# Kernel tuning notes

Hardware: AMD Instinct MI355X
Metric: run time of the kernel (lower is better)

The kernel has to match this reference:

```python
import jax, jax.numpy as jnp
import numpy as np

B, S, D = 1, 2048, 1024
H = 16            # num_heads
DH = D // H       # head dim = 64
WIN = 128         # local window size
DIL = 4           # dilation rate


def setup_inputs() -> dict:
    key = jax.random.key(0)
    k1, k2, k3 = jax.random.split(key, 3)
    x = jax.random.normal(k1, (B, S, D), jnp.float32)
    w_qkv = jax.random.normal(k2, (D, 3 * D), jnp.float32) * 0.02
    w_out = jax.random.normal(k3, (D, D), jnp.float32) * 0.02
    return {"x": x, "w_qkv": w_qkv, "w_out": w_out}


def reference(x, w_qkv, w_out):
    b, s, d = x.shape
    scale = 1.0 / np.sqrt(DH).astype(np.float32)

    qkv = x @ w_qkv                                   # [B,S,3D]
    q, k, v = jnp.split(qkv, 3, axis=-1)
    q = q.reshape(b, s, H, DH)
    k = k.reshape(b, s, H, DH)
    v = v.reshape(b, s, H, DH)

    # ---- local window attention: attend within non-overlapping windows ----
    nw = s // WIN
    qw = q.reshape(b, nw, WIN, H, DH)
    kw = k.reshape(b, nw, WIN, H, DH)
    vw = v.reshape(b, nw, WIN, H, DH)
    s_loc = jnp.einsum('bnihd,bnjhd->bnhij', qw, kw) * scale
    p_loc = jax.nn.softmax(s_loc, axis=-1)
    o_loc = jnp.einsum('bnhij,bnjhd->bnihd', p_loc, vw).reshape(b, s, H, DH)

    # ---- dilated attention: attend within each stride-DIL residue class ----
    n = s // DIL
    # seq index = i*DIL + g  -> position i within dilation group g
    qd = q.reshape(b, n, DIL, H, DH)
    kd = k.reshape(b, n, DIL, H, DH)
    vd = v.reshape(b, n, DIL, H, DH)
    s_dil = jnp.einsum('bighd,bjghd->bghij', qd, kd) * scale
    p_dil = jax.nn.softmax(s_dil, axis=-1)
    o_dil = jnp.einsum('bghij,bjghd->bighd', p_dil, vd).reshape(b, s, H, DH)

    # ---- global full attention ----
    s_glb = jnp.einsum('bihd,bjhd->bhij', q, k) * scale
    p_glb = jax.nn.softmax(s_glb, axis=-1)
    o_glb = jnp.einsum('bhij,bjhd->bihd', p_glb, v)

    # fuse the three scales (uniform average) and project out
    o = (o_loc + o_dil + o_glb) * (1.0 / 3.0)
    return o.reshape(b, s, d) @ w_out
```

## Files before the change

kernel.cpp:

```cpp
#include <hip/hip_runtime.h>
#include <hip/hip_bf16.h>


typedef __attribute__((ext_vector_type(8))) short s8v;
typedef __attribute__((ext_vector_type(4))) float f4v;

#define QSCALE 0.18033688011112042f

__device__ __forceinline__ short f2bf(float f) {
  union { float f; unsigned u; } x; x.f = f;
  unsigned r = (x.u + 0x7FFF + ((x.u >> 16) & 1)) >> 16;
  return (short)r;
}
__device__ __forceinline__ float bf2f(short s) {
  union { unsigned u; float f; } x; x.u = ((unsigned)(unsigned short)s) << 16;
  return x.f;
}
__device__ __forceinline__ f4v mfma16(s8v a, s8v b, f4v c) {
  return __builtin_amdgcn_mfma_f32_16x16x32_bf16(a, b, c, 0, 0, 0);
}
__device__ __forceinline__ void load_lds16(const void* g, void* l) {
  __builtin_amdgcn_global_load_lds(
      (const __attribute__((address_space(1))) unsigned int*)g,
      (__attribute__((address_space(3))) unsigned int*)l, 16, 0, 0);
}
__device__ __forceinline__ float exp2f_fast(float x) {
  return __builtin_amdgcn_exp2f(x);
}

__global__ __launch_bounds__(256)
void fill_const_kernel(float* __restrict__ out, int n, float v) {
  int i = blockIdx.x * 256 + threadIdx.x;
  if (i < n) out[i] = v;
}

__global__ __launch_bounds__(256)
void cast_f32_bf16(const float* __restrict__ src, short* __restrict__ dst, int n) {
  int i = (blockIdx.x * 256 + threadIdx.x) * 4;
  if (i < n) {
    float4 v = *reinterpret_cast<const float4*>(&src[i]);
    union { short s[4]; int2 p; } u;
    u.s[0] = f2bf(v.x); u.s[1] = f2bf(v.y); u.s[2] = f2bf(v.z); u.s[3] = f2bf(v.w);
    *reinterpret_cast<int2*>(&dst[i]) = u.p;
  }
}

__global__ __launch_bounds__(256)
void transpose_conv(const float* __restrict__ src, short* __restrict__ dst,
                    int K, int N) {
  __shared__ float T[64][69];
  const int n0 = blockIdx.x * 64, k0 = blockIdx.y * 64;
  const int t = threadIdx.x;
  for (int jb = t; jb < 1024; jb += 256) {
    int r = jb >> 4, c4 = (jb & 15) * 4;
    float4 v = *reinterpret_cast<const float4*>(&src[(size_t)(k0 + r) * N + n0 + c4]);
    T[c4 + 0][r] = v.x; T[c4 + 1][r] = v.y; T[c4 + 2][r] = v.z; T[c4 + 3][r] = v.w;
  }
  __syncthreads();
  for (int jb = t; jb < 512; jb += 256) {
    int n = jb >> 3, k8 = (jb & 7) * 8;
    union { short s[8]; int4 v; } p;
#pragma unroll
    for (int i = 0; i < 8; ++i) p.s[i] = f2bf(T[n][k8 + i]);
    *reinterpret_cast<int4*>(&dst[(size_t)(n0 + n) * K + k0 + k8]) = p.v;
  }
}

template <int COUT, bool AF32, int NT>
__global__ __launch_bounds__(256)
void gemm_tile(const void* __restrict__ Av, const short* __restrict__ Bt,
               short* __restrict__ qb, short* __restrict__ kb,
               short* __restrict__ vT, float* __restrict__ co,
               int K, int N) {
  __shared__ __align__(16) short As[64 * 32];
  __shared__ __align__(16) short Bs[NT * 32];
  const int tid = threadIdx.x, wave = tid >> 6;
  const int li = tid & 63;
  const int row0 = blockIdx.y * 64, col0 = blockIdx.x * NT;
  const int lr = li & 15, quad = li >> 4, lk = quad * 8;
  constexpr int NTW = NT / 64;

  f4v acc[4][NTW];
#pragma unroll
  for (int i = 0; i < 4; ++i)
#pragma unroll
    for (int j = 0; j < NTW; ++j) acc[i][j] = (f4v){0.f, 0.f, 0.f, 0.f};

  for (int k0 = 0; k0 < K; k0 += 32) {
    __syncthreads();
#pragma unroll
    for (int u = 0; u < NTW; ++u)
      load_lds16(Bt + (size_t)(col0 + u * 64 + (tid >> 2)) * K + k0 + (tid & 3) * 8,
                 &Bs[u * 2048 + wave * 512]);
    if (AF32) {
      const float* A = (const float*)Av;
#pragma unroll
      for (int c = 0; c < 2; ++c) {
        int j = c * 256 + tid;
        int r = j >> 3, c4 = (j & 7) * 4;
        float4 v = *reinterpret_cast<const float4*>(&A[(size_t)(row0 + r) * K + k0 + c4]);
        union { short s[4]; int2 v2; } p;
        p.s[0] = f2bf(v.x); p.s[1] = f2bf(v.y); p.s[2] = f2bf(v.z); p.s[3] = f2bf(v.w);
        *reinterpret_cast<int2*>(&As[r * 32 + c4]) = p.v2;
      }
    } else {
      load_lds16((const short*)Av + (size_t)(row0 + (tid >> 2)) * K + k0 + (tid & 3) * 8,
                 &As[wave * 512]);
    }
    __syncthreads();

    s8v af[4], bfr[NTW];
#pragma unroll
    for (int mt = 0; mt < 4; ++mt)
      af[mt] = *reinterpret_cast<const s8v*>(&As[(mt * 16 + lr) * 32 + lk]);
#pragma unroll
    for (int u = 0; u < NTW; ++u)
      bfr[u] = *reinterpret_cast<const s8v*>(&Bs[(wave * (NT / 4) + u * 16 + lr) * 32 + lk]);
#pragma unroll
    for (int mt = 0; mt < 4; ++mt)
#pragma unroll
      for (int u = 0; u < NTW; ++u)
        acc[mt][u] = mfma16(af[mt], bfr[u], acc[mt][u]);
  }

#pragma unroll
  for (int mt = 0; mt < 4; ++mt) {
#pragma unroll
    for (int u = 0; u < NTW; ++u) {
      int gcol = col0 + wave * (NT / 4) + u * 16 + lr;
      int grow0 = row0 + mt * 16 + quad * 4;
      if (COUT == 0) {
        if (gcol >= 2048) {
          int d = gcol - 2048;
          int j = grow0 >> 2;
          int k64 = j & 63;
          int gb = ((j >> 6) << 6) + ((k64 >> 5) << 5) +
                   ((k64 & 7) << 2) + ((k64 >> 3) & 3);
          size_t base = (size_t)d * 2048 + gb;
#pragma unroll
          for (int r = 0; r < 4; ++r)
            vT[base + (r << 9)] = f2bf(acc[mt][u][r]);
        } else {
          short* dst = (gcol < 1024) ? qb : kb;
          float sc = (gcol < 1024) ? QSCALE : 1.0f;
          int c = gcol & 1023;
#pragma unroll
          for (int r = 0; r < 4; ++r)
            dst[(size_t)(grow0 + r) * 1024 + c] = f2bf(acc[mt][u][r] * sc);
        }
      } else {
#pragma unroll
        for (int r = 0; r < 4; ++r)
          co[(size_t)(grow0 + r) * N + gcol] = acc[mt][u][r] * (1.0f / 3.0f);
      }
    }
  }
}

__global__ __launch_bounds__(256, 2)
void attn_unified(const short* __restrict__ qb, const short* __restrict__ kb,
                  const short* __restrict__ vT, short* __restrict__ o) {
  __shared__ __align__(16) short Qs[64][72];
  __shared__ __align__(16) short Ks[2][64][72];
  __shared__ __align__(16) short Vt[2][64][72];
  __shared__ __align__(16) short Pls[64][72];

  const int tid = threadIdx.x;
  const int wave = tid >> 6, li = tid & 63;
  const int b = blockIdx.x, h = b & 15, g = b >> 4;
  const int qcol = h * 64;
  const int lr = li & 15, quad = li >> 4, lk = quad * 8;
  const int wt2 = g >> 2;
  const int wH  = (g >> 1) & 1;
  const bool wlane = ((lr >> 3) == wH);

  for (int jb = tid; jb < 512; jb += 256) {
    int r = jb >> 3, c8 = (jb & 7) * 8;
    *reinterpret_cast<int4*>(&Qs[r][c8]) =
        *reinterpret_cast<const int4*>(&qb[(size_t)(g * 64 + r) * 1024 + qcol + c8]);
  }
#pragma unroll
  for (int c = 0; c < 2; ++c) {
    int j = c * 256 + tid;
    int r = j >> 3, c8 = (j & 7) * 8;
    int k64 = ((r & 8) << 2) + ((r >> 4) << 3) + (r & 7);
    *reinterpret_cast<int4*>(&Ks[0][r][c8]) =
        *reinterpret_cast<const int4*>(&kb[(size_t)(k64 << 2) * 1024 + qcol + c8]);
    *reinterpret_cast<int4*>(&Vt[0][r][c8]) =
        *reinterpret_cast<const int4*>(&vT[(size_t)(h * 64 + r) * 2048 + c8]);
  }
  __syncthreads();

  float l_r[4]   = {0.f, 0.f, 0.f, 0.f};
  float l_loc[4] = {0.f, 0.f, 0.f, 0.f};
  float l_dil[4] = {0.f, 0.f, 0.f, 0.f};
  float lsnap[4];
  f4v oacc[4], o_loc[4], o_dil[4], snapd[4];
#pragma unroll
  for (int i = 0; i < 4; ++i) {
    oacc[i]  = (f4v){0.f, 0.f, 0.f, 0.f};
    o_loc[i] = (f4v){0.f, 0.f, 0.f, 0.f};
    o_dil[i] = (f4v){0.f, 0.f, 0.f, 0.f};
  }

  for (int t = 0; t < 32; ++t) {
    const int cur = t & 1, nxt = cur ^ 1;
    const bool pf = (t + 1 < 32);
    const bool wtile = ((t & 7) == wt2);

    if ((t & 7) == 0) {
#pragma unroll
      for (int i = 0; i < 4; ++i) { snapd[i] = oacc[i]; lsnap[i] = l_r[i]; }
    }

    int4 kpre[2], vpre[2];
    if (pf) {
#pragma unroll
      for (int c = 0; c < 2; ++c) {
        int j = c * 256 + tid;
        int r = j >> 3, c8 = (j & 7) * 8;
        int k64 = ((r & 8) << 2) + ((r >> 4) << 3) + (r & 7);
        int ks = ((((t + 1) & 7) << 6) + k64) * 4 + ((t + 1) >> 3);
        kpre[c] = *reinterpret_cast<const int4*>(&kb[(size_t)ks * 1024 + qcol + c8]);
        vpre[c] = *reinterpret_cast<const int4*>(
            &vT[(size_t)(h * 64 + r) * 2048 + (t + 1) * 64 + c8]);
      }
    }

    f4v s4[4];
#pragma unroll
    for (int i = 0; i < 4; ++i) s4[i] = (f4v){0.f, 0.f, 0.f, 0.f};
#pragma unroll
    for (int ks2 = 0; ks2 < 2; ++ks2) {
      s8v aq = *reinterpret_cast<const s8v*>(&Qs[wave * 16 + lr][ks2 * 32 + lk]);
#pragma unroll
      for (int nt = 0; nt < 4; ++nt) {
        s8v bk = *reinterpret_cast<const s8v*>(&Ks[cur][nt * 16 + lr][ks2 * 32 + lk]);
        s4[nt] = mfma16(aq, bk, s4[nt]);
      }
    }

#pragma unroll
    for (int r = 0; r < 4; ++r) {
      float p0 = exp2f_fast(s4[0][r]), p1 = exp2f_fast(s4[1][r]),
            p2 = exp2f_fast(s4[2][r]), p3 = exp2f_fast(s4[3][r]);
      float ps = (p0 + p1) + (p2 + p3);
      l_r[r] += ps;
      l_loc[r] += (wtile && wlane) ? ps : 0.f;
      union { short s[4]; int2 v; } pk;
      pk.s[0] = f2bf(p0); pk.s[1] = f2bf(p1); pk.s[2] = f2bf(p2); pk.s[3] = f2bf(p3);
      *reinterpret_cast<int2*>(&Pls[wave * 16 + quad * 4 + r][4 * lr]) = pk.v;
    }

#pragma unroll
    for (int ks2 = 0; ks2 < 2; ++ks2) {
      s8v ap = *reinterpret_cast<const s8v*>(&Pls[wave * 16 + lr][ks2 * 32 + lk]);
      bool sh = wtile && (wH == ks2);
      if (sh) {
#pragma unroll
        for (int nt = 0; nt < 4; ++nt) {
          s8v bv = *reinterpret_cast<const s8v*>(&Vt[cur][nt * 16 + lr][ks2 * 32 + lk]);
          f4v dd = mfma16(ap, bv, (f4v){0.f, 0.f, 0.f, 0.f});
          oacc[nt] += dd;
          o_loc[nt] += dd;
        }
      } else {
#pragma unroll
        for (int nt = 0; nt < 4; ++nt) {
          s8v bv = *reinterpret_cast<const s8v*>(&Vt[cur][nt * 16 + lr][ks2 * 32 + lk]);
          oacc[nt] = mfma16(ap, bv, oacc[nt]);
        }
      }
    }

    if ((t & 7) == 7) {
      const int rho = t >> 3;
#pragma unroll
      for (int i = 0; i < 4; ++i) {
        float m = (i == rho) ? 1.f : 0.f;
        l_dil[i] += m * (l_r[i] - lsnap[i]);
#pragma unroll
        for (int nt = 0; nt < 4; ++nt)
          o_dil[nt][i] += m * (oacc[nt][i] - snapd[nt][i]);
      }
    }

    if (pf) {
#pragma unroll
      for (int c = 0; c < 2; ++c) {
        int j = c * 256 + tid;
        int r = j >> 3, c8 = (j & 7) * 8;
        *reinterpret_cast<int4*>(&Ks[nxt][r][c8]) = kpre[c];
        *reinterpret_cast<int4*>(&Vt[nxt][r][c8]) = vpre[c];
      }
    }
    __syncthreads();
  }

#pragma unroll
  for (int r = 0; r < 4; ++r) {
    float lg = l_r[r], ll = l_loc[r], ld = l_dil[r];
    lg += __shfl_xor(lg, 1, 16);  ll += __shfl_xor(ll, 1, 16);  ld += __shfl_xor(ld, 1, 16);
    lg += __shfl_xor(lg, 2, 16);  ll += __shfl_xor(ll, 2, 16);  ld += __shfl_xor(ld, 2, 16);
    lg += __shfl_xor(lg, 4, 16);  ll += __shfl_xor(ll, 4, 16);  ld += __shfl_xor(ld, 4, 16);
    lg += __shfl_xor(lg, 8, 16);  ll += __shfl_xor(ll, 8, 16);  ld += __shfl_xor(ld, 8, 16);
    float ig = 1.0f / lg, il = 1.0f / ll, id = 1.0f / ld;
    int rowt = wave * 16 + quad * 4 + r;
    int qs = g * 64 + rowt;
#pragma unroll
    for (int nt = 0; nt < 4; ++nt) {
      size_t idx = (size_t)qs * 1024 + qcol + nt * 16 + lr;
      o[idx] = f2bf(oacc[nt][r] * ig + o_loc[nt][r] * il + o_dil[nt][r] * id);
    }
  }
}

extern "C" void kernel_launch(void* const* d_in, const int* in_sizes, int n_in,
                              void* d_out, int out_size, void* d_ws, size_t ws_size,
                              hipStream_t stream) {
  float* out = (float*)d_out;
  const int nfill = (out_size + 255) / 256;
  if (n_in != 3) { fill_const_kernel<<<nfill, 256, 0, stream>>>(out, out_size, 0.5f); return; }
  int ix = -1, iq = -1, io = -1;
  for (int i = 0; i < 3; ++i) {
    if      (in_sizes[i] == 2097152) ix = i;
    else if (in_sizes[i] == 3145728) iq = i;
    else if (in_sizes[i] == 1048576) io = i;
  }
  if (ix < 0 || iq < 0 || io < 0) { fill_const_kernel<<<nfill, 256, 0, stream>>>(out, out_size, 0.3f); return; }
  const float* x     = (const float*)d_in[ix];
  const float* w_qkv = (const float*)d_in[iq];
  const float* w_out = (const float*)d_in[io];

  char* ws = (char*)d_ws;
  const size_t MB = 1048576;
  const size_t needX = 22 * MB;
  const size_t needY = 20 * MB;

  if (ws_size >= needX) {
    short* qb     = (short*)(ws);
    short* kb     = (short*)(ws + 4 * MB);
    short* vT     = (short*)(ws + 8 * MB);
    short* w_qkvT = (short*)(ws + 12 * MB);
    short* xb     = (short*)(ws + 18 * MB);
    short* o      = (short*)(ws + 12 * MB);
    short* w_outT = (short*)(ws + 16 * MB);
    cast_f32_bf16<<<2048, 256, 0, stream>>>(x, xb, 2097152);
    transpose_conv<<<dim3(48, 16), 256, 0, stream>>>(w_qkv, w_qkvT, 1024, 3072);
    gemm_tile<0, false, 128><<<dim3(24, 32), 256, 0, stream>>>(xb, w_qkvT, qb, kb, vT, nullptr, 1024, 3072);
    transpose_conv<<<dim3(16, 16), 256, 0, stream>>>(w_out, w_outT, 1024, 1024);
    attn_unified<<<512, 256, 0, stream>>>(qb, kb, vT, o);
    gemm_tile<1, false, 64><<<dim3(16, 32), 256, 0, stream>>>(o, w_outT, nullptr, nullptr, nullptr, out, 1024, 1024);
  } else if (ws_size >= needY) {
    short* w_outT = (short*)(ws);
    short* qb     = (short*)(ws + 2 * MB);
    short* kb     = (short*)(ws + 6 * MB);
    short* vT     = (short*)(ws + 10 * MB);
    short* w_qkvT = (short*)(ws + 14 * MB);
    short* o      = (short*)(ws + 14 * MB);
    transpose_conv<<<dim3(48, 16), 256, 0, stream>>>(w_qkv, w_qkvT, 1024, 3072);
    transpose_conv<<<dim3(16, 16), 256, 0, stream>>>(w_out, w_outT, 1024, 1024);
    gemm_tile<0, true, 128><<<dim3(24, 32), 256, 0, stream>>>(x, w_qkvT, qb, kb, vT, nullptr, 1024, 3072);
    attn_unified<<<512, 256, 0, stream>>>(qb, kb, vT, o);
    gemm_tile<1, false, 64><<<dim3(16, 32), 256, 0, stream>>>(o, w_outT, nullptr, nullptr, nullptr, out, 1024, 1024);
  } else {
    fill_const_kernel<<<nfill, 256, 0, stream>>>(out, out_size, 0.2f);
  }
}
```

Baseline: 162.4 us.

## Split attention key tiles across two wave groups with 512-thread blocks

The attention kernel doubles its block to 512 threads. The two 4-wave groups each handle half of every 64-key tile, and their partial outputs and row sums are combined through LDS at the end. Q fragments stay in registers instead of a shared tile. The V-transpose permutation in the QKV GEMM epilogue changes to match the new key-half ownership, and the dilation snapshots move into an unrolled rho loop instead of masked per-step updates. This is meant to raise parallelism and cut per-wave serial MFMA work, at the cost of a cross-group reduction, extra syncs and higher register pressure from launch_bounds(512,4).

```diff
diff --git a/kernel.cpp b/kernel.cpp
--- a/kernel.cpp
+++ b/kernel.cpp
@@ -11,10 +11,6 @@
   union { float f; unsigned u; } x; x.f = f;
   unsigned r = (x.u + 0x7FFF + ((x.u >> 16) & 1)) >> 16;
   return (short)r;
-}
-__device__ __forceinline__ float bf2f(short s) {
-  union { unsigned u; float f; } x; x.u = ((unsigned)(unsigned short)s) << 16;
-  return x.f;
 }
 __device__ __forceinline__ f4v mfma16(s8v a, s8v b, f4v c) {
   return __builtin_amdgcn_mfma_f32_16x16x32_bf16(a, b, c, 0, 0, 0);
@@ -133,9 +129,8 @@
         if (gcol >= 2048) {
           int d = gcol - 2048;
           int j = grow0 >> 2;
-          int k64 = j & 63;
-          int gb = ((j >> 6) << 6) + ((k64 >> 5) << 5) +
-                   ((k64 & 7) << 2) + ((k64 >> 3) & 3);
+          int gb = ((j >> 6) << 6) + (((j >> 5) & 1) << 5) +
+                   ((j & 15) << 1) + ((j >> 4) & 1);
           size_t base = (size_t)d * 2048 + gb;
 #pragma unroll
           for (int r = 0; r < 4; ++r)
@@ -157,45 +152,42 @@
   }
 }
 
-__global__ __launch_bounds__(256, 2)
+__global__ __launch_bounds__(512, 4)
 void attn_unified(const short* __restrict__ qb, const short* __restrict__ kb,
                   const short* __restrict__ vT, short* __restrict__ o) {
-  __shared__ __align__(16) short Qs[64][72];
   __shared__ __align__(16) short Ks[2][64][72];
   __shared__ __align__(16) short Vt[2][64][72];
-  __shared__ __align__(16) short Pls[64][72];
+  __shared__ __align__(16) short Pls[8][16][40];
+  __shared__ float lX[2][4][4][12];
 
   const int tid = threadIdx.x;
   const int wave = tid >> 6, li = tid & 63;
+  const int grp = wave >> 2, wr = wave & 3;
   const int b = blockIdx.x, h = b & 15, g = b >> 4;
   const int qcol = h * 64;
   const int lr = li & 15, quad = li >> 4, lk = quad * 8;
   const int wt2 = g >> 2;
   const int wH  = (g >> 1) & 1;
-  const bool wlane = ((lr >> 3) == wH);
-
-  for (int jb = tid; jb < 512; jb += 256) {
-    int r = jb >> 3, c8 = (jb & 7) * 8;
-    *reinterpret_cast<int4*>(&Qs[r][c8]) =
-        *reinterpret_cast<const int4*>(&qb[(size_t)(g * 64 + r) * 1024 + qcol + c8]);
-  }
-#pragma unroll
-  for (int c = 0; c < 2; ++c) {
-    int j = c * 256 + tid;
-    int r = j >> 3, c8 = (j & 7) * 8;
-    int k64 = ((r & 8) << 2) + ((r >> 4) << 3) + (r & 7);
-    *reinterpret_cast<int4*>(&Ks[0][r][c8]) =
-        *reinterpret_cast<const int4*>(&kb[(size_t)(k64 << 2) * 1024 + qcol + c8]);
-    *reinterpret_cast<int4*>(&Vt[0][r][c8]) =
-        *reinterpret_cast<const int4*>(&vT[(size_t)(h * 64 + r) * 2048 + c8]);
-  }
+  const bool wgrp = (grp == wH);
+  const int sr = tid >> 3, sc8 = (tid & 7) * 8;
+
+  s8v q0, q1;
+  {
+    const short* qrow = &qb[(size_t)(g * 64 + wr * 16 + lr) * 1024 + qcol];
+    q0 = *reinterpret_cast<const s8v*>(&qrow[lk]);
+    q1 = *reinterpret_cast<const s8v*>(&qrow[32 + lk]);
+  }
+
+  *reinterpret_cast<int4*>(&Ks[0][sr][sc8]) =
+      *reinterpret_cast<const int4*>(&kb[(size_t)(sr << 2) * 1024 + qcol + sc8]);
+  *reinterpret_cast<int4*>(&Vt[0][sr][sc8]) =
+      *reinterpret_cast<const int4*>(&vT[(size_t)(h * 64 + sr) * 2048 + sc8]);
   __syncthreads();
 
   float l_r[4]   = {0.f, 0.f, 0.f, 0.f};
   float l_loc[4] = {0.f, 0.f, 0.f, 0.f};
   float l_dil[4] = {0.f, 0.f, 0.f, 0.f};
-  float lsnap[4];
-  f4v oacc[4], o_loc[4], o_dil[4], snapd[4];
+  f4v oacc[4], o_loc[4], o_dil[4];
 #pragma unroll
   for (int i = 0; i < 4; ++i) {
     oacc[i]  = (f4v){0.f, 0.f, 0.f, 0.f};
@@ -203,114 +195,142 @@
     o_dil[i] = (f4v){0.f, 0.f, 0.f, 0.f};
   }
 
-  for (int t = 0; t < 32; ++t) {
-    const int cur = t & 1, nxt = cur ^ 1;
-    const bool pf = (t + 1 < 32);
-    const bool wtile = ((t & 7) == wt2);
-
-    if ((t & 7) == 0) {
-#pragma unroll
-      for (int i = 0; i < 4; ++i) { snapd[i] = oacc[i]; lsnap[i] = l_r[i]; }
+  const int koffA = ((grp * 2 + 0) * 16 + lr) * 72 + lk;
+  const int koffB = ((grp * 2 + 1) * 16 + lr) * 72 + lk;
+  const short* KsF = &Ks[0][0][0];
+  const short* VtF = &Vt[0][0][0];
+
+#pragma unroll
+  for (int rho = 0; rho < 4; ++rho) {
+    const float sn0 = oacc[0][rho], sn1 = oacc[1][rho],
+                sn2 = oacc[2][rho], sn3 = oacc[3][rho];
+    const float lsn = l_r[rho];
+
+#pragma unroll 2
+    for (int t8 = 0; t8 < 8; ++t8) {
+      const int t = rho * 8 + t8;
+      const int cur = t8 & 1, nxt = cur ^ 1;
+      const bool pf = (rho < 3) || (t8 < 7);
+      const bool wt = wgrp && (t8 == wt2);
+      const int cb = cur * 4608;
+
+      int4 kpre, vpre;
+      if (pf) {
+        const int tn = t + 1;
+        const int ksn = ((((tn & 7) << 6) + sr) << 2) + (tn >> 3);
+        kpre = *reinterpret_cast<const int4*>(&kb[(size_t)ksn * 1024 + qcol + sc8]);
+        vpre = *reinterpret_cast<const int4*>(
+            &vT[(size_t)(h * 64 + sr) * 2048 + tn * 64 + sc8]);
+      }
+
+      f4v s4a = (f4v){0.f, 0.f, 0.f, 0.f};
+      f4v s4b = (f4v){0.f, 0.f, 0.f, 0.f};
+      s4a = mfma16(q0, *reinterpret_cast<const s8v*>(&KsF[cb + koffA]), s4a);
+      s4b = mfma16(q0, *reinterpret_cast<const s8v*>(&KsF[cb + koffB]), s4b);
+      s4a = mfma16(q1, *reinterpret_cast<const s8v*>(&KsF[cb + koffA + 32]), s4a);
+      s4b = mfma16(q1, *reinterpret_cast<const s8v*>(&KsF[cb + koffB + 32]), s4b);
+
+#pragma unroll
+      for (int r = 0; r < 4; ++r) {
+        float p0 = exp2f_fast(s4a[r]), p1 = exp2f_fast(s4b[r]);
+        float ps = p0 + p1;
+        l_r[r] += ps;
+        if (wt) l_loc[r] += ps;
+        union { short s[2]; int v; } pk;
+        pk.s[0] = f2bf(p0); pk.s[1] = f2bf(p1);
+        *reinterpret_cast<int*>(&Pls[wave][quad * 4 + r][2 * lr]) = pk.v;
+      }
+
+      {
+        s8v ap = *reinterpret_cast<const s8v*>(&Pls[wave][lr][lk]);
+        if (wt) {
+#pragma unroll
+          for (int nt = 0; nt < 4; ++nt) {
+            s8v bv = *reinterpret_cast<const s8v*>(
+                &VtF[cb + (nt * 16 + lr) * 72 + grp * 32 + lk]);
+            f4v dd = mfma16(ap, bv, (f4v){0.f, 0.f, 0.f, 0.f});
+            oacc[nt] += dd;
+            o_loc[nt] += dd;
+          }
+        } else {
+#pragma unroll
+          for (int nt = 0; nt < 4; ++nt) {
+            s8v bv = *reinterpret_cast<const s8v*>(
+                &VtF[cb + (nt * 16 + lr) * 72 + grp * 32 + lk]);
+            oacc[nt] = mfma16(ap, bv, oacc[nt]);
+          }
+        }
+      }
+
+      if (pf) {
+        *reinterpret_cast<int4*>(&Ks[nxt][sr][sc8]) = kpre;
+        *reinterpret_cast<int4*>(&Vt[nxt][sr][sc8]) = vpre;
+      }
+      __syncthreads();
     }
 
-    int4 kpre[2], vpre[2];
-    if (pf) {
-#pragma unroll
-      for (int c = 0; c < 2; ++c) {
-        int j = c * 256 + tid;
-        int r = j >> 3, c8 = (j & 7) * 8;
-        int k64 = ((r & 8) << 2) + ((r >> 4) << 3) + (r & 7);
-        int ks = ((((t + 1) & 7) << 6) + k64) * 4 + ((t + 1) >> 3);
-        kpre[c] = *reinterpret_cast<const int4*>(&kb[(size_t)ks * 1024 + qcol + c8]);
-        vpre[c] = *reinterpret_cast<const int4*>(
-            &vT[(size_t)(h * 64 + r) * 2048 + (t + 1) * 64 + c8]);
-      }
-    }
-
-    f4v s4[4];
-#pragma unroll
-    for (int i = 0; i < 4; ++i) s4[i] = (f4v){0.f, 0.f, 0.f, 0.f};
-#pragma unroll
-    for (int ks2 = 0; ks2 < 2; ++ks2) {
-      s8v aq = *reinterpret_cast<const s8v*>(&Qs[wave * 16 + lr][ks2 * 32 + lk]);
-#pragma unroll
-      for (int nt = 0; nt < 4; ++nt) {
-        s8v bk = *reinterpret_cast<const s8v*>(&Ks[cur][nt * 16 + lr][ks2 * 32 + lk]);
-        s4[nt] = mfma16(aq, bk, s4[nt]);
-      }
-    }
-
+    l_dil[rho] = l_r[rho] - lsn;
+    o_dil[0][rho] = oacc[0][rho] - sn0;
+    o_dil[1][rho] = oacc[1][rho] - sn1;
+    o_dil[2][rho] = oacc[2][rho] - sn2;
+    o_dil[3][rho] = oacc[3][rho] - sn3;
+  }
+
+  float lv[12];
+#pragma unroll
+  for (int r = 0; r < 4; ++r) { lv[r] = l_r[r]; lv[4 + r] = l_loc[r]; lv[8 + r] = l_dil[r]; }
+#pragma unroll
+  for (int k = 0; k < 12; ++k) {
+    lv[k] += __shfl_xor(lv[k], 1, 16);
+    lv[k] += __shfl_xor(lv[k], 2, 16);
+    lv[k] += __shfl_xor(lv[k], 4, 16);
+    lv[k] += __shfl_xor(lv[k], 8, 16);
+  }
+  if (lr == 0) {
+#pragma unroll
+    for (int k = 0; k < 12; ++k) lX[grp][wr][quad][k] = lv[k];
+  }
+  __syncthreads();
+
+  f4v part[4];
+#pragma unroll
+  for (int r = 0; r < 4; ++r) {
+    float lg = lX[0][wr][quad][r]     + lX[1][wr][quad][r];
+    float ll = lX[0][wr][quad][4 + r] + lX[1][wr][quad][4 + r];
+    float ld = lX[0][wr][quad][8 + r] + lX[1][wr][quad][8 + r];
+    float ig = 1.0f / lg, il = 1.0f / ll, id = 1.0f / ld;
+#pragma unroll
+    for (int nt = 0; nt < 4; ++nt)
+      part[nt][r] = oacc[nt][r] * ig + o_loc[nt][r] * il + o_dil[nt][r] * id;
+  }
+
+  float* xch = reinterpret_cast<float*>(&Ks[0][0][0]);
+  const int slot = wr * 64 + li;
+  if (grp == 1) {
+#pragma unroll
+    for (int nt = 0; nt < 4; ++nt)
+#pragma unroll
+      for (int hh = 0; hh < 2; ++hh) {
+        float2 v2 = make_float2(part[nt][2 * hh], part[nt][2 * hh + 1]);
+        *reinterpret_cast<float2*>(&xch[slot * 18 + (nt * 2 + hh) * 2]) = v2;
+      }
+  }
+  __syncthreads();
+  if (grp == 0) {
+#pragma unroll
+    for (int nt = 0; nt < 4; ++nt)
+#pragma unroll
+      for (int hh = 0; hh < 2; ++hh) {
+        float2 v2 = *reinterpret_cast<const float2*>(&xch[slot * 18 + (nt * 2 + hh) * 2]);
+        part[nt][2 * hh]     += v2.x;
+        part[nt][2 * hh + 1] += v2.y;
+      }
 #pragma unroll
     for (int r = 0; r < 4; ++r) {
-      float p0 = exp2f_fast(s4[0][r]), p1 = exp2f_fast(s4[1][r]),
-            p2 = exp2f_fast(s4[2][r]), p3 = exp2f_fast(s4[3][r]);
-      float ps = (p0 + p1) + (p2 + p3);
-      l_r[r] += ps;
-      l_loc[r] += (wtile && wlane) ? ps : 0.f;
-      union { short s[4]; int2 v; } pk;
-      pk.s[0] = f2bf(p0); pk.s[1] = f2bf(p1); pk.s[2] = f2bf(p2); pk.s[3] = f2bf(p3);
-      *reinterpret_cast<int2*>(&Pls[wave * 16 + quad * 4 + r][4 * lr]) = pk.v;
-    }
-
-#pragma unroll
-    for (int ks2 = 0; ks2 < 2; ++ks2) {
-      s8v ap = *reinterpret_cast<const s8v*>(&Pls[wave * 16 + lr][ks2 * 32 + lk]);
-      bool sh = wtile && (wH == ks2);
-      if (sh) {
-#pragma unroll
-        for (int nt = 0; nt < 4; ++nt) {
-          s8v bv = *reinterpret_cast<const s8v*>(&Vt[cur][nt * 16 + lr][ks2 * 32 + lk]);
-          f4v dd = mfma16(ap, bv, (f4v){0.f, 0.f, 0.f, 0.f});
-          oacc[nt] += dd;
-          o_loc[nt] += dd;
-        }
-      } else {
-#pragma unroll
-        for (int nt = 0; nt < 4; ++nt) {
-          s8v bv = *reinterpret_cast<const s8v*>(&Vt[cur][nt * 16 + lr][ks2 * 32 + lk]);
-          oacc[nt] = mfma16(ap, bv, oacc[nt]);
-        }
-      }
-    }
-
-    if ((t & 7) == 7) {
-      const int rho = t >> 3;
-#pragma unroll
-      for (int i = 0; i < 4; ++i) {
-        float m = (i == rho) ? 1.f : 0.f;
-        l_dil[i] += m * (l_r[i] - lsnap[i]);
-#pragma unroll
-        for (int nt = 0; nt < 4; ++nt)
-          o_dil[nt][i] += m * (oacc[nt][i] - snapd[nt][i]);
-      }
-    }
-
-    if (pf) {
-#pragma unroll
-      for (int c = 0; c < 2; ++c) {
-        int j = c * 256 + tid;
-        int r = j >> 3, c8 = (j & 7) * 8;
-        *reinterpret_cast<int4*>(&Ks[nxt][r][c8]) = kpre[c];
-        *reinterpret_cast<int4*>(&Vt[nxt][r][c8]) = vpre[c];
-      }
-    }
-    __syncthreads();
-  }
-
-#pragma unroll
-  for (int r = 0; r < 4; ++r) {
-    float lg = l_r[r], ll = l_loc[r], ld = l_dil[r];
-    lg += __shfl_xor(lg, 1, 16);  ll += __shfl_xor(ll, 1, 16);  ld += __shfl_xor(ld, 1, 16);
-    lg += __shfl_xor(lg, 2, 16);  ll += __shfl_xor(ll, 2, 16);  ld += __shfl_xor(ld, 2, 16);
-    lg += __shfl_xor(lg, 4, 16);  ll += __shfl_xor(ll, 4, 16);  ld += __shfl_xor(ld, 4, 16);
-    lg += __shfl_xor(lg, 8, 16);  ll += __shfl_xor(ll, 8, 16);  ld += __shfl_xor(ld, 8, 16);
-    float ig = 1.0f / lg, il = 1.0f / ll, id = 1.0f / ld;
-    int rowt = wave * 16 + quad * 4 + r;
-    int qs = g * 64 + rowt;
-#pragma unroll
-    for (int nt = 0; nt < 4; ++nt) {
-      size_t idx = (size_t)qs * 1024 + qcol + nt * 16 + lr;
-      o[idx] = f2bf(oacc[nt][r] * ig + o_loc[nt][r] * il + o_dil[nt][r] * id);
+      int qs = g * 64 + wr * 16 + quad * 4 + r;
+#pragma unroll
+      for (int nt = 0; nt < 4; ++nt)
+        o[(size_t)qs * 1024 + qcol + nt * 16 + lr] = f2bf(part[nt][r]);
     }
   }
 }
@@ -349,7 +369,7 @@
     transpose_conv<<<dim3(48, 16), 256, 0, stream>>>(w_qkv, w_qkvT, 1024, 3072);
     gemm_tile<0, false, 128><<<dim3(24, 32), 256, 0, stream>>>(xb, w_qkvT, qb, kb, vT, nullptr, 1024, 3072);
     transpose_conv<<<dim3(16, 16), 256, 0, stream>>>(w_out, w_outT, 1024, 1024);
-    attn_unified<<<512, 256, 0, stream>>>(qb, kb, vT, o);
+    attn_unified<<<512, 512, 0, stream>>>(qb, kb, vT, o);
     gemm_tile<1, false, 64><<<dim3(16, 32), 256, 0, stream>>>(o, w_outT, nullptr, nullptr, nullptr, out, 1024, 1024);
   } else if (ws_size >= needY) {
     short* w_outT = (short*)(ws);
@@ -361,7 +381,7 @@
     transpose_conv<<<dim3(48, 16), 256, 0, stream>>>(w_qkv, w_qkvT, 1024, 3072);
     transpose_conv<<<dim3(16, 16), 256, 0, stream>>>(w_out, w_outT, 1024, 1024);
     gemm_tile<0, true, 128><<<dim3(24, 32), 256, 0, stream>>>(x, w_qkvT, qb, kb, vT, nullptr, 1024, 3072);
-    attn_unified<<<512, 256, 0, stream>>>(qb, kb, vT, o);
+    attn_unified<<<512, 512, 0, stream>>>(qb, kb, vT, o);
     gemm_tile<1, false, 64><<<dim3(16, 32), 256, 0, stream>>>(o, w_outT, nullptr, nullptr, nullptr, out, 1024, 1024);
   } else {
     fill_const_kernel<<<nfill, 256, 0, stream>>>(out, out_size, 0.2f);
```

After: 172.1 us. 1.06x slower.
